# Performance work log

Hardware: AMD Instinct MI355X
Metric: run time of the kernel (lower is better)

The kernel has to match this reference:

```python
import jax, jax.numpy as jnp
import numpy as np

C_RGLRU = 8.0

def _rg_lru(x, wa, ba, wx, bx, lam):
    # x: [B, L, D]. Griffin RG-LRU (De et al. 2024).
    r = jax.nn.sigmoid(jnp.einsum('bld,ed->ble', x, wa) + ba)
    i = jax.nn.sigmoid(jnp.einsum('bld,ed->ble', x, wx) + bx)
    log_a = -C_RGLRU * r * jax.nn.softplus(lam)          # [B,L,D], <= 0
    a = jnp.exp(log_a)
    mult = jnp.sqrt(jnp.maximum(1.0 - jnp.exp(2.0 * log_a), 0.0))
    b = mult * (i * x)
    def combine(c1, c2):
        a1, b1 = c1
        a2, b2 = c2
        return a1 * a2, a2 * b1 + b2
    _, h = jax.lax.associative_scan(combine, (a, b), axis=1)
    return h

def setup_inputs() -> dict:
    key = jax.random.key(0)
    ks = jax.random.split(key, 12)
    B, L, D, R = 4, 2048, 2048, 2560
    s_d = 1.0 / np.sqrt(D)
    s_r = 1.0 / np.sqrt(R)
    s_c = 1.0 / np.sqrt(R * 4)
    return {
        'x':      jax.random.normal(ks[0], (B, L, D), jnp.float32),
        'w1':     jax.random.normal(ks[1], (R, D), jnp.float32) * s_d,
        'b1':     jnp.zeros((R,), jnp.float32),
        'conv_w': jax.random.normal(ks[2], (R, R, 4), jnp.float32) * s_c,
        'conv_b': jnp.zeros((R,), jnp.float32),
        'wa':     jax.random.normal(ks[3], (R, R), jnp.float32) * s_r,
        'ba':     jnp.zeros((R,), jnp.float32),
        'wx':     jax.random.normal(ks[4], (R, R), jnp.float32) * s_r,
        'bx':     jnp.zeros((R,), jnp.float32),
        'lam':    jax.random.uniform(ks[5], (R,), jnp.float32, 0.5, 2.0),
        'w2':     jax.random.normal(ks[6], (D, R), jnp.float32) * s_r,
        'b2':     jnp.zeros((D,), jnp.float32),
    }

def reference(x, w1, b1, conv_w, conv_b, wa, ba, wx, bx, lam, w2, b2):
    # linear1 + SiLU: [B,L,D] -> [B,L,R]
    h = jax.nn.silu(jnp.einsum('bld,rd->blr', x, w1) + b1)
    # temporal conv1d: kernel 4, dilation 2, padding 3 both sides (as in torch)
    hc = h.transpose(0, 2, 1)  # [B,R,L]
    hc = jax.lax.conv_general_dilated(
        hc, conv_w, window_strides=(1,), padding=[(3, 3)],
        rhs_dilation=(2,), dimension_numbers=('NCH', 'OIH', 'NCH'))
    hc = hc + conv_b[None, :, None]
    h = hc.transpose(0, 2, 1)  # [B,L,R]
    # RG-LRU gated linear recurrence
    h = _rg_lru(h, wa, ba, wx, bx, lam)
    # linear2: [B,L,R] -> [B,L,D]
    return jnp.einsum('blr,dr->bld', h, w2) + b2
```

## Files before the change

kernel.cpp:

```cpp
#include <hip/hip_runtime.h>

#define B_  4
#define L_  2048
#define D_  2048
#define R_  2560
#define BL_ (B_ * L_)

#define CHK_  16
#define CLEN_ (L_ / CHK_)

typedef unsigned short u16;
typedef unsigned int   u32;

typedef __attribute__((ext_vector_type(8))) short short8;
typedef __attribute__((ext_vector_type(4))) float f32x4;
typedef __attribute__((ext_vector_type(4))) int   int4v;

static __device__ __forceinline__ u16 f2bf(float f) {
  u32 x = __float_as_uint(f);
  x += 0x7fffu + ((x >> 16) & 1u);
  return (u16)(x >> 16);
}
static __device__ __forceinline__ float bf2f(u16 u) {
  return __uint_as_float(((u32)u) << 16);
}

static __device__ __forceinline__ void gld16(const u16* g, u16* l) {
  __builtin_amdgcn_global_load_lds(
      (const __attribute__((address_space(1))) void*)g,
      (__attribute__((address_space(3))) void*)l, 16, 0, 0);
}

__global__ void cvt_bf16(const float* __restrict__ src, u16* __restrict__ dst, int n) {
  int i = blockIdx.x * blockDim.x + threadIdx.x;
  int stride = gridDim.x * blockDim.x;
  for (; i < n; i += stride) dst[i] = f2bf(src[i]);
}

__global__ void cvt_convw(const float* __restrict__ cw, u16* __restrict__ out) {
  int i = blockIdx.x * blockDim.x + threadIdx.x;
  if (i >= R_ * R_) return;
  const float4 v = *(const float4*)(cw + (size_t)i * 4);
  out[(size_t)0 * R_ * R_ + i] = f2bf(v.x);
  out[(size_t)1 * R_ * R_ + i] = f2bf(v.y);
  out[(size_t)2 * R_ * R_ + i] = f2bf(v.z);
  out[(size_t)3 * R_ * R_ + i] = f2bf(v.w);
}

template <int ACT , int OBF16 >
__global__ __launch_bounds__(256)
void gemm_bt(const u16* __restrict__ A, const u16* __restrict__ Bm,
             const float* __restrict__ bias, void* __restrict__ Cv,
             int M, int N, int K) {
  __shared__ u16 As[128 * 32];
  __shared__ u16 Bs[128 * 32];
  const int tid  = threadIdx.x;
  const int bm   = blockIdx.x * 128, bn = blockIdx.y * 128;
  const int wave = tid >> 6, lane = tid & 63;
  const int wm   = (wave >> 1) * 64, wn = (wave & 1) * 64;
  const int q    = lane >> 4, r16 = lane & 15;
  const int lrow = lane >> 2;
  const int gch  = (lane & 3) ^ (lrow & 3);

  f32x4 acc[4][4] = {};

  const int swz = (q ^ (r16 & 3)) * 8;

  for (int kk = 0; kk < K; kk += 32) {
#pragma unroll
    for (int p = 0; p < 2; ++p) {
      const int rb = wave * 32 + p * 16;
      gld16(A  + (size_t)(bm + rb + lrow) * K + kk + gch * 8, &As[rb * 32]);
      gld16(Bm + (size_t)(bn + rb + lrow) * K + kk + gch * 8, &Bs[rb * 32]);
    }
    __syncthreads();
    short8 af[4], bfr[4];
#pragma unroll
    for (int i = 0; i < 4; ++i)
      af[i] = *(const short8*)(&As[(wm + i * 16 + r16) * 32 + swz]);
#pragma unroll
    for (int j = 0; j < 4; ++j)
      bfr[j] = *(const short8*)(&Bs[(wn + j * 16 + r16) * 32 + swz]);
#pragma unroll
    for (int i = 0; i < 4; ++i)
#pragma unroll
      for (int j = 0; j < 4; ++j)
        acc[i][j] = __builtin_amdgcn_mfma_f32_16x16x32_bf16(af[i], bfr[j], acc[i][j], 0, 0, 0);
    __syncthreads();
  }

#pragma unroll
  for (int i = 0; i < 4; ++i) {
    const int row = bm + wm + i * 16 + q * 4;
#pragma unroll
    for (int j = 0; j < 4; ++j) {
      const int col = bn + wn + j * 16 + r16;
      const float bv = bias[col];
#pragma unroll
      for (int rr = 0; rr < 4; ++rr) {
        float v = acc[i][j][rr] + bv;
        if (ACT == 1) v = v / (1.f + __expf(-v));
        const size_t off = (size_t)(row + rr) * N + col;
        if (OBF16) ((u16*)Cv)[off] = f2bf(v);
        else       ((float*)Cv)[off] = v;
      }
    }
  }
}

__global__ __launch_bounds__(256)
void conv_gemm(const u16* __restrict__ A, const u16* __restrict__ CW,
               const float* __restrict__ bias, u16* __restrict__ C) {
  __shared__ u16 As[128 * 32];
  __shared__ u16 Bs[128 * 32];
  const int tid  = threadIdx.x;
  const int bm   = blockIdx.x * 128, bn = blockIdx.y * 128;
  const int wave = tid >> 6, lane = tid & 63;
  const int wm   = (wave >> 1) * 64, wn = (wave & 1) * 64;
  const int q    = lane >> 4, r16 = lane & 15;
  const int lrow = lane >> 2;
  const int gch  = (lane & 3) ^ (lrow & 3);
  const int swz  = (q ^ (r16 & 3)) * 8;
  const int r0 = tid >> 2, c0g = (tid & 3) * 8;
  const int dsw0 = ((tid & 3) ^ (r0 & 3)) * 8;
  const int l0 = (bm + r0) & (L_ - 1), l1 = (bm + r0 + 64) & (L_ - 1);
  const int tileL = blockIdx.x & 15;

  f32x4 acc[4][4] = {};

  for (int tap = 0; tap < 4; ++tap) {
    const int sh = 2 * tap - 3;
    const bool safe = (sh < 0) ? (tileL != 0) : (tileL != 15);
    const bool v0 = (unsigned)(l0 + sh) < (unsigned)L_;
    const bool v1 = (unsigned)(l1 + sh) < (unsigned)L_;
    const u16* aSh = A + (ptrdiff_t)(bm + sh) * R_;
    const u16* bp  = CW + (size_t)tap * R_ * R_;
    const int4v zz = {0, 0, 0, 0};
    for (int kk = 0; kk < R_; kk += 32) {
#pragma unroll
      for (int p = 0; p < 2; ++p) {
        const int rb = wave * 32 + p * 16;
        gld16(bp + (size_t)(bn + rb + lrow) * R_ + kk + gch * 8, &Bs[rb * 32]);
      }
      if (safe) {
#pragma unroll
        for (int p = 0; p < 2; ++p) {
          const int rb = wave * 32 + p * 16;
          gld16(aSh + (size_t)(rb + lrow) * R_ + kk + gch * 8, &As[rb * 32]);
        }
      } else {
        *(int4v*)(&As[r0 * 32 + dsw0]) =
            v0 ? *(const int4v*)(aSh + (size_t)r0 * R_ + kk + c0g) : zz;
        *(int4v*)(&As[(r0 + 64) * 32 + dsw0]) =
            v1 ? *(const int4v*)(aSh + (size_t)(r0 + 64) * R_ + kk + c0g) : zz;
      }
      __syncthreads();
      short8 af[4], bfr[4];
#pragma unroll
      for (int i = 0; i < 4; ++i)
        af[i] = *(const short8*)(&As[(wm + i * 16 + r16) * 32 + swz]);
#pragma unroll
      for (int j = 0; j < 4; ++j)
        bfr[j] = *(const short8*)(&Bs[(wn + j * 16 + r16) * 32 + swz]);
#pragma unroll
      for (int i = 0; i < 4; ++i)
#pragma unroll
        for (int j = 0; j < 4; ++j)
          acc[i][j] = __builtin_amdgcn_mfma_f32_16x16x32_bf16(af[i], bfr[j], acc[i][j], 0, 0, 0);
      __syncthreads();
    }
  }

#pragma unroll
  for (int i = 0; i < 4; ++i) {
    const int row = bm + wm + i * 16 + q * 4;
#pragma unroll
    for (int j = 0; j < 4; ++j) {
      const int col = bn + wn + j * 16 + r16;
      const float bv = bias[col];
#pragma unroll
      for (int rr = 0; rr < 4; ++rr) {
        float v = acc[i][j][rr] + bv;
        C[(size_t)(row + rr) * R_ + col] = f2bf(v);
      }
    }
  }
}

__global__ void gate_ew(const u16* __restrict__ gab, const u16* __restrict__ gib,
                        const u16* __restrict__ h2b, const float* __restrict__ lam,
                        float* __restrict__ a32, float* __restrict__ b32) {
  int idx = blockIdx.x * blockDim.x + threadIdx.x;
  if (idx >= BL_ * R_) return;
  const int r = idx % R_;
  const float ga = bf2f(gab[idx]);
  const float gi = bf2f(gib[idx]);
  const float h2 = bf2f(h2b[idx]);
  const float rr = 1.f / (1.f + __expf(-ga));
  const float ii = 1.f / (1.f + __expf(-gi));
  const float lm = lam[r];
  const float sp = log1pf(__expf(lm));
  const float log_a = -8.f * rr * sp;
  const float a  = __expf(log_a);
  const float e2 = __expf(2.f * log_a);
  const float mult = sqrtf(fmaxf(1.f - e2, 0.f));
  a32[idx] = a;
  b32[idx] = mult * ii * h2;
}

__global__ void scan_pass1(const float* __restrict__ a32, const float* __restrict__ b32,
                           float* __restrict__ Aprod, float* __restrict__ Hend) {
  int t = blockIdx.x * blockDim.x + threadIdx.x;
  if (t >= CHK_ * B_ * R_) return;
  const int c = t / (B_ * R_), br = t % (B_ * R_);
  const int b = br / R_, r = br % R_;
  size_t idx = ((size_t)b * L_ + c * CLEN_) * R_ + r;
  float Ap = 1.f, h = 0.f;
  for (int l = 0; l < CLEN_; ++l) {
    const float a = a32[idx], bb = b32[idx];
    Ap *= a;
    h = a * h + bb;
    idx += R_;
  }
  Aprod[t] = Ap;
  Hend[t]  = h;
}

__global__ void scan_pass2(const float* __restrict__ Aprod, float* __restrict__ Hend) {
  int br = blockIdx.x * blockDim.x + threadIdx.x;
  if (br >= B_ * R_) return;
  float h = Hend[br];
  for (int c = 1; c < CHK_; ++c) {
    const int i = c * (B_ * R_) + br;
    h = Hend[i] + Aprod[i] * h;
    Hend[i] = h;
  }
}

__global__ void scan_pass3(const float* __restrict__ a32, const float* __restrict__ b32,
                           const float* __restrict__ Hend, u16* __restrict__ hs) {
  int t = blockIdx.x * blockDim.x + threadIdx.x;
  if (t >= CHK_ * B_ * R_) return;
  const int c = t / (B_ * R_), br = t % (B_ * R_);
  const int b = br / R_, r = br % R_;
  float h = (c == 0) ? 0.f : Hend[(size_t)(c - 1) * (B_ * R_) + br];
  size_t idx = ((size_t)b * L_ + c * CLEN_) * R_ + r;
  for (int l = 0; l < CLEN_; ++l) {
    h = a32[idx] * h + b32[idx];
    hs[idx] = f2bf(h);
    idx += R_;
  }
}

extern "C" void kernel_launch(void* const* d_in, const int* in_sizes, int n_in,
                              void* d_out, int out_size, void* d_ws, size_t ws_size,
                              hipStream_t stream) {
  (void)in_sizes; (void)n_in; (void)out_size; (void)ws_size;
  const float* x   = (const float*)d_in[0];
  const float* w1  = (const float*)d_in[1];
  const float* b1  = (const float*)d_in[2];
  const float* cw  = (const float*)d_in[3];
  const float* cb  = (const float*)d_in[4];
  const float* wa  = (const float*)d_in[5];
  const float* ba  = (const float*)d_in[6];
  const float* wx  = (const float*)d_in[7];
  const float* bx  = (const float*)d_in[8];
  const float* lam = (const float*)d_in[9];
  const float* w2  = (const float*)d_in[10];
  const float* b2  = (const float*)d_in[11];

  char* ws = (char*)d_ws;
  size_t o = 0;
  auto alloc = [&](size_t bytes) { char* p = ws + o; o += (bytes + 255) & ~255ull; return p; };

  u16* w2b = (u16*)alloc((size_t)D_ * R_ * 2);
  u16* wab = (u16*)alloc((size_t)R_ * R_ * 2);
  u16* wxb = (u16*)alloc((size_t)R_ * R_ * 2);
  char* a32p = ws + o;
  u16* xb  = (u16*)alloc((size_t)BL_ * D_ * 2);
  u16* w1b = (u16*)alloc((size_t)R_ * D_ * 2);
  u16* cwb = (u16*)alloc((size_t)4 * R_ * R_ * 2);
  char* b32p = ws + o;
  u16* h1b = (u16*)alloc((size_t)BL_ * R_ * 2);
  alloc((size_t)BL_ * R_ * 2);
  u16* h2b = (u16*)alloc((size_t)BL_ * R_ * 2);
  u16* gab = (u16*)alloc((size_t)BL_ * R_ * 2);
  u16* gib = (u16*)alloc((size_t)BL_ * R_ * 2);
  float* Aprod = (float*)alloc((size_t)CHK_ * B_ * R_ * 4);
  float* Hend  = (float*)alloc((size_t)CHK_ * B_ * R_ * 4);
  float* a32 = (float*)a32p;
  float* b32 = (float*)b32p;
  u16* hsb = gab;

  cvt_bf16<<<4096, 256, 0, stream>>>(x,  xb,  BL_ * D_);
  cvt_bf16<<<2048, 256, 0, stream>>>(w1, w1b, R_ * D_);
  cvt_bf16<<<2048, 256, 0, stream>>>(wa, wab, R_ * R_);
  cvt_bf16<<<2048, 256, 0, stream>>>(wx, wxb, R_ * R_);
  cvt_bf16<<<2048, 256, 0, stream>>>(w2, w2b, D_ * R_);
  cvt_convw<<<(R_ * R_ + 255) / 256, 256, 0, stream>>>(cw, cwb);

  gemm_bt<1, 1><<<dim3(BL_ / 128, R_ / 128), 256, 0, stream>>>(xb, w1b, b1, h1b, BL_, R_, D_);
  conv_gemm<<<dim3(BL_ / 128, R_ / 128), 256, 0, stream>>>(h1b, cwb, cb, h2b);
  gemm_bt<0, 1><<<dim3(BL_ / 128, R_ / 128), 256, 0, stream>>>(h2b, wab, ba, gab, BL_, R_, R_);
  gemm_bt<0, 1><<<dim3(BL_ / 128, R_ / 128), 256, 0, stream>>>(h2b, wxb, bx, gib, BL_, R_, R_);
  gate_ew<<<(BL_ * R_ + 255) / 256, 256, 0, stream>>>(gab, gib, h2b, lam, a32, b32);
  scan_pass1<<<(CHK_ * B_ * R_ + 255) / 256, 256, 0, stream>>>(a32, b32, Aprod, Hend);
  scan_pass2<<<(B_ * R_ + 255) / 256, 256, 0, stream>>>(Aprod, Hend);
  scan_pass3<<<(CHK_ * B_ * R_ + 255) / 256, 256, 0, stream>>>(a32, b32, Hend, hsb);
  gemm_bt<0, 0><<<dim3(BL_ / 128, D_ / 128), 256, 0, stream>>>(hsb, w2b, b2, d_out, BL_, D_, R_);
}
```

Measured before the change: 1.643 ms.

## Share halo A tile across conv taps and fuse gating into scan passes

The conv GEMM now loads one 136-row A tile per K-step, including a halo, and reuses it for all four taps by shifting the row index. It loads the four tap weight tiles together into shared memory, so each K-step needs two barriers instead of eight. Separately, the elementwise gate kernel is removed and the gating math is recomputed inside scan pass 1 and pass 3 from bf16 inputs. This avoids writing and re-reading the fp32 a/b arrays, at the cost of repeating the transcendental math in both passes. The conv change uses more LDS and drops the async direct-to-LDS path for A in favour of register-staged loads.

```diff
diff --git a/kernel.cpp b/kernel.cpp
--- a/kernel.cpp
+++ b/kernel.cpp
@@ -111,8 +111,8 @@
 __global__ __launch_bounds__(256)
 void conv_gemm(const u16* __restrict__ A, const u16* __restrict__ CW,
                const float* __restrict__ bias, u16* __restrict__ C) {
-  __shared__ u16 As[128 * 32];
-  __shared__ u16 Bs[128 * 32];
+  __shared__ u16 As[136 * 32];
+  __shared__ u16 Bs[4][128 * 32];
   const int tid  = threadIdx.x;
   const int bm   = blockIdx.x * 128, bn = blockIdx.y * 128;
   const int wave = tid >> 6, lane = tid & 63;
@@ -120,55 +120,59 @@
   const int q    = lane >> 4, r16 = lane & 15;
   const int lrow = lane >> 2;
   const int gch  = (lane & 3) ^ (lrow & 3);
-  const int swz  = (q ^ (r16 & 3)) * 8;
-  const int r0 = tid >> 2, c0g = (tid & 3) * 8;
-  const int dsw0 = ((tid & 3) ^ (r0 & 3)) * 8;
-  const int l0 = (bm + r0) & (L_ - 1), l1 = (bm + r0 + 64) & (L_ - 1);
+  const int swzB = (q ^ (r16 & 3)) * 8;
   const int tileL = blockIdx.x & 15;
 
+  const u16* aptr[3]; int aoff[3]; bool aval[3], ado[3];
+  for (int u = 0; u < 3; ++u) {
+    const int c   = tid + u * 256;
+    const int row = c >> 2, s = c & 3;
+    const int gc  = s ^ (row & 3);
+    ado[u]  = (c < 536);
+    const int lrel = tileL * 128 - 3 + row;
+    aval[u] = ado[u] && ((unsigned)lrel < (unsigned)L_);
+    aoff[u] = ado[u] ? (row * 32 + s * 8) : 0;
+    aptr[u] = A + (size_t)(bm - 3 + row) * R_ + gc * 8;
+  }
+
   f32x4 acc[4][4] = {};
-
-  for (int tap = 0; tap < 4; ++tap) {
-    const int sh = 2 * tap - 3;
-    const bool safe = (sh < 0) ? (tileL != 0) : (tileL != 15);
-    const bool v0 = (unsigned)(l0 + sh) < (unsigned)L_;
-    const bool v1 = (unsigned)(l1 + sh) < (unsigned)L_;
-    const u16* aSh = A + (ptrdiff_t)(bm + sh) * R_;
-    const u16* bp  = CW + (size_t)tap * R_ * R_;
-    const int4v zz = {0, 0, 0, 0};
-    for (int kk = 0; kk < R_; kk += 32) {
+  const int4v zz = {0, 0, 0, 0};
+
+  for (int kk = 0; kk < R_; kk += 32) {
+#pragma unroll
+    for (int tap = 0; tap < 4; ++tap)
 #pragma unroll
       for (int p = 0; p < 2; ++p) {
         const int rb = wave * 32 + p * 16;
-        gld16(bp + (size_t)(bn + rb + lrow) * R_ + kk + gch * 8, &Bs[rb * 32]);
-      }
-      if (safe) {
-#pragma unroll
-        for (int p = 0; p < 2; ++p) {
-          const int rb = wave * 32 + p * 16;
-          gld16(aSh + (size_t)(rb + lrow) * R_ + kk + gch * 8, &As[rb * 32]);
-        }
-      } else {
-        *(int4v*)(&As[r0 * 32 + dsw0]) =
-            v0 ? *(const int4v*)(aSh + (size_t)r0 * R_ + kk + c0g) : zz;
-        *(int4v*)(&As[(r0 + 64) * 32 + dsw0]) =
-            v1 ? *(const int4v*)(aSh + (size_t)(r0 + 64) * R_ + kk + c0g) : zz;
-      }
-      __syncthreads();
+        gld16(CW + ((size_t)tap * R_ + (size_t)(bn + rb + lrow)) * R_ + kk + gch * 8,
+              &Bs[tap][rb * 32]);
+      }
+#pragma unroll
+    for (int u = 0; u < 3; ++u)
+      if (ado[u]) {
+        const int4v v = aval[u] ? *(const int4v*)(aptr[u] + kk) : zz;
+        *(int4v*)(&As[aoff[u]]) = v;
+      }
+    __syncthreads();
+#pragma unroll
+    for (int tap = 0; tap < 4; ++tap) {
+      const int shoff = 2 * tap;
       short8 af[4], bfr[4];
 #pragma unroll
-      for (int i = 0; i < 4; ++i)
-        af[i] = *(const short8*)(&As[(wm + i * 16 + r16) * 32 + swz]);
+      for (int i = 0; i < 4; ++i) {
+        const int rowa = wm + i * 16 + r16 + shoff;
+        af[i] = *(const short8*)(&As[rowa * 32 + ((q ^ (rowa & 3)) * 8)]);
+      }
 #pragma unroll
       for (int j = 0; j < 4; ++j)
-        bfr[j] = *(const short8*)(&Bs[(wn + j * 16 + r16) * 32 + swz]);
+        bfr[j] = *(const short8*)(&Bs[tap][(wn + j * 16 + r16) * 32 + swzB]);
 #pragma unroll
       for (int i = 0; i < 4; ++i)
 #pragma unroll
         for (int j = 0; j < 4; ++j)
           acc[i][j] = __builtin_amdgcn_mfma_f32_16x16x32_bf16(af[i], bfr[j], acc[i][j], 0, 0, 0);
-      __syncthreads();
     }
+    __syncthreads();
   }
 
 #pragma unroll
@@ -187,37 +191,29 @@
   }
 }
 
-__global__ void gate_ew(const u16* __restrict__ gab, const u16* __restrict__ gib,
-                        const u16* __restrict__ h2b, const float* __restrict__ lam,
-                        float* __restrict__ a32, float* __restrict__ b32) {
-  int idx = blockIdx.x * blockDim.x + threadIdx.x;
-  if (idx >= BL_ * R_) return;
-  const int r = idx % R_;
-  const float ga = bf2f(gab[idx]);
-  const float gi = bf2f(gib[idx]);
-  const float h2 = bf2f(h2b[idx]);
-  const float rr = 1.f / (1.f + __expf(-ga));
-  const float ii = 1.f / (1.f + __expf(-gi));
-  const float lm = lam[r];
-  const float sp = log1pf(__expf(lm));
+static __device__ __forceinline__ void gate_ab(u16 ga, u16 gi, u16 h2, float sp,
+                                               float& a, float& bb) {
+  const float rr = 1.f / (1.f + __expf(-bf2f(ga)));
+  const float ii = 1.f / (1.f + __expf(-bf2f(gi)));
   const float log_a = -8.f * rr * sp;
-  const float a  = __expf(log_a);
+  a = __expf(log_a);
   const float e2 = __expf(2.f * log_a);
-  const float mult = sqrtf(fmaxf(1.f - e2, 0.f));
-  a32[idx] = a;
-  b32[idx] = mult * ii * h2;
-}
-
-__global__ void scan_pass1(const float* __restrict__ a32, const float* __restrict__ b32,
+  bb = sqrtf(fmaxf(1.f - e2, 0.f)) * ii * bf2f(h2);
+}
+
+__global__ void scan_pass1(const u16* __restrict__ gab, const u16* __restrict__ gib,
+                           const u16* __restrict__ h2b, const float* __restrict__ lam,
                            float* __restrict__ Aprod, float* __restrict__ Hend) {
   int t = blockIdx.x * blockDim.x + threadIdx.x;
   if (t >= CHK_ * B_ * R_) return;
   const int c = t / (B_ * R_), br = t % (B_ * R_);
   const int b = br / R_, r = br % R_;
+  const float sp = log1pf(__expf(lam[r]));
   size_t idx = ((size_t)b * L_ + c * CLEN_) * R_ + r;
   float Ap = 1.f, h = 0.f;
   for (int l = 0; l < CLEN_; ++l) {
-    const float a = a32[idx], bb = b32[idx];
+    float a, bb;
+    gate_ab(gab[idx], gib[idx], h2b[idx], sp, a, bb);
     Ap *= a;
     h = a * h + bb;
     idx += R_;
@@ -237,16 +233,20 @@
   }
 }
 
-__global__ void scan_pass3(const float* __restrict__ a32, const float* __restrict__ b32,
+__global__ void scan_pass3(const u16* __restrict__ gab, const u16* __restrict__ gib,
+                           const u16* __restrict__ h2b, const float* __restrict__ lam,
                            const float* __restrict__ Hend, u16* __restrict__ hs) {
   int t = blockIdx.x * blockDim.x + threadIdx.x;
   if (t >= CHK_ * B_ * R_) return;
   const int c = t / (B_ * R_), br = t % (B_ * R_);
   const int b = br / R_, r = br % R_;
+  const float sp = log1pf(__expf(lam[r]));
   float h = (c == 0) ? 0.f : Hend[(size_t)(c - 1) * (B_ * R_) + br];
   size_t idx = ((size_t)b * L_ + c * CLEN_) * R_ + r;
   for (int l = 0; l < CLEN_; ++l) {
-    h = a32[idx] * h + b32[idx];
+    float a, bb;
+    gate_ab(gab[idx], gib[idx], h2b[idx], sp, a, bb);
+    h = a * h + bb;
     hs[idx] = f2bf(h);
     idx += R_;
   }
@@ -276,20 +276,15 @@
   u16* w2b = (u16*)alloc((size_t)D_ * R_ * 2);
   u16* wab = (u16*)alloc((size_t)R_ * R_ * 2);
   u16* wxb = (u16*)alloc((size_t)R_ * R_ * 2);
-  char* a32p = ws + o;
   u16* xb  = (u16*)alloc((size_t)BL_ * D_ * 2);
   u16* w1b = (u16*)alloc((size_t)R_ * D_ * 2);
   u16* cwb = (u16*)alloc((size_t)4 * R_ * R_ * 2);
-  char* b32p = ws + o;
   u16* h1b = (u16*)alloc((size_t)BL_ * R_ * 2);
-  alloc((size_t)BL_ * R_ * 2);
   u16* h2b = (u16*)alloc((size_t)BL_ * R_ * 2);
   u16* gab = (u16*)alloc((size_t)BL_ * R_ * 2);
   u16* gib = (u16*)alloc((size_t)BL_ * R_ * 2);
   float* Aprod = (float*)alloc((size_t)CHK_ * B_ * R_ * 4);
   float* Hend  = (float*)alloc((size_t)CHK_ * B_ * R_ * 4);
-  float* a32 = (float*)a32p;
-  float* b32 = (float*)b32p;
   u16* hsb = gab;
 
   cvt_bf16<<<4096, 256, 0, stream>>>(x,  xb,  BL_ * D_);
@@ -303,9 +298,8 @@
   conv_gemm<<<dim3(BL_ / 128, R_ / 128), 256, 0, stream>>>(h1b, cwb, cb, h2b);
   gemm_bt<0, 1><<<dim3(BL_ / 128, R_ / 128), 256, 0, stream>>>(h2b, wab, ba, gab, BL_, R_, R_);
   gemm_bt<0, 1><<<dim3(BL_ / 128, R_ / 128), 256, 0, stream>>>(h2b, wxb, bx, gib, BL_, R_, R_);
-  gate_ew<<<(BL_ * R_ + 255) / 256, 256, 0, stream>>>(gab, gib, h2b, lam, a32, b32);
-  scan_pass1<<<(CHK_ * B_ * R_ + 255) / 256, 256, 0, stream>>>(a32, b32, Aprod, Hend);
+  scan_pass1<<<(CHK_ * B_ * R_ + 255) / 256, 256, 0, stream>>>(gab, gib, h2b, lam, Aprod, Hend);
   scan_pass2<<<(B_ * R_ + 255) / 256, 256, 0, stream>>>(Aprod, Hend);
-  scan_pass3<<<(CHK_ * B_ * R_ + 255) / 256, 256, 0, stream>>>(a32, b32, Hend, hsb);
+  scan_pass3<<<(CHK_ * B_ * R_ + 255) / 256, 256, 0, stream>>>(gab, gib, h2b, lam, Hend, hsb);
   gemm_bt<0, 0><<<dim3(BL_ / 128, D_ / 128), 256, 0, stream>>>(hsb, w2b, b2, d_out, BL_, D_, R_);
 }
```

Result: slower. 1.679 ms (+2.2%).
